# Optimization experiments

Hardware: AMD Instinct MI355X
Metric: run time of the kernel (lower is better)

The kernel has to match this reference:

```python
import jax, jax.numpy as jnp
import numpy as np

N_INST = 64
H, W_SP = 200, 320


def setup_inputs() -> dict:
    key = jax.random.key(0)
    ks = jax.random.split(key, 10)
    mask = jax.random.normal(ks[0], (1, N_INST, H, W_SP), dtype=jnp.float32)
    # class indices must lie in [1, 80]
    cls_idx = jax.random.randint(ks[1], (N_INST,), 0, 80, dtype=jnp.int32) + 1
    # rois: [batch_idx, xmin, ymin, xmax, ymax] with positive w, h
    xmin = jax.random.uniform(ks[2], (N_INST,), dtype=jnp.float32) * 800.0
    ymin = jax.random.uniform(ks[3], (N_INST,), dtype=jnp.float32) * 600.0
    bw = jax.random.uniform(ks[4], (N_INST,), dtype=jnp.float32) * 200.0 + 2.0
    bh = jax.random.uniform(ks[5], (N_INST,), dtype=jnp.float32) * 200.0 + 2.0
    bbox = jnp.stack([jnp.zeros(N_INST, jnp.float32), xmin, ymin, xmin + bw - 1.0, ymin + bh - 1.0], axis=1)
    # parameters (kaiming-ish scaling)
    U_w = jax.random.normal(ks[6], (256, 80), dtype=jnp.float32) * (2.0 / 80.0) ** 0.5
    V_w = jax.random.normal(ks[7], (256, 80), dtype=jnp.float32) * (2.0 / 80.0) ** 0.5
    Wc_w = jax.random.normal(ks[8], (128, 4), dtype=jnp.float32) * (2.0 / 4.0) ** 0.5
    P_w = jax.random.normal(ks[9], (1, 384), dtype=jnp.float32) * (2.0 / 384.0) ** 0.5
    return {"mask": mask, "bbox": bbox, "cls_idx": cls_idx,
            "U_w": U_w, "V_w": V_w, "Wc_w": Wc_w, "P_w": P_w}


def _position_matrix(rois):
    xmin, ymin, xmax, ymax = rois[:, 1], rois[:, 2], rois[:, 3], rois[:, 4]
    w = xmax - xmin + 1.0
    h = ymax - ymin + 1.0
    x_ctr = xmin + 0.5 * w
    y_ctr = ymin + 0.5 * h
    dx = -(x_ctr[:, None] - x_ctr[None, :]) / w[:, None]
    dy = -(y_ctr[:, None] - y_ctr[None, :]) / h[:, None]
    dw = jnp.log(w[None, :] / w[:, None])
    dh = jnp.log(h[None, :] / h[:, None])
    return jnp.stack([dx, dy, dw, dh], axis=2)  # (N, N, 4)


def reference(mask, bbox, cls_idx, U_w, V_w, Wc_w, P_w):
    n = cls_idx.shape[0]
    onehot = (cls_idx[:, None] - 1 == jnp.arange(80)[None, :]).astype(jnp.float32)  # (N, 80)
    feat1 = jax.nn.relu(onehot @ U_w.T)  # (N, 256)
    feat2 = jax.nn.relu(onehot @ V_w.T)  # (N, 256)
    cls_rel = feat1[:, None, :] * feat2[None, :, :]  # (N, N, 256)
    bbox_mat = _position_matrix(bbox)  # (N, N, 4)
    bbox_feat = jax.nn.relu(jnp.einsum('ijc,oc->ijo', bbox_mat, Wc_w))  # (N, N, 128)
    feat = jnp.concatenate([cls_rel, bbox_feat], axis=2)  # (N, N, 384)
    logit = jnp.einsum('ijc,c->ij', feat, P_w[0])  # 1x1 conv to scalar
    R = jax.nn.sigmoid(logit)
    O = jax.nn.relu(R - R.T)  # (N, N)
    trans_mask = jax.nn.sigmoid(mask)  # (1, N, H, W)
    # overlap[0,i] = mask[0,i]*trans_mask[0,i] * sum_j O[i,j]*trans_mask[0,j]
    weighted = jnp.einsum('ij,bjhw->bihw', O, trans_mask)
    new_mask = mask - mask * trans_mask * weighted
    return new_mask, O
```

## Files before the change

### kernel.cpp

```cpp
#include <hip/hip_runtime.h>
#include <math.h>

#define N_INST 64
#define HW 64000
#define TP 64
#define MASK_BLOCKS (HW / TP)

__device__ __forceinline__ float sigmoidf_(float x) {
    return 1.0f / (1.0f + __expf(-x));
}


__global__ void k_gather(const int* __restrict__ cls,
                         const float* __restrict__ U_w,
                         const float* __restrict__ V_w,
                         const float* __restrict__ P_w,
                         float* __restrict__ Afp,
                         float* __restrict__ BfT) {
    const int b = blockIdx.x;
    const int tid = threadIdx.x;
    const int cb = cls[b] - 1;
    float u = U_w[tid * 80 + cb];
    Afp[b * 256 + tid] = fmaxf(u, 0.0f) * P_w[tid];
    const int c = b * 4 + (tid >> 6);
    const int j = tid & 63;
    const int cj = cls[j] - 1;
    float v = V_w[c * 80 + cj];
    BfT[c * 64 + j] = fmaxf(v, 0.0f);
}

__global__ __launch_bounds__(64) void k_pair(const float* __restrict__ bbox,
                                             const float* __restrict__ Afp,
                                             const float* __restrict__ BfT,
                                             const float* __restrict__ Wc_w,
                                             const float* __restrict__ P_w,
                                             float* __restrict__ logit) {
    const int i = blockIdx.x;
    const int j = threadIdx.x;

    const float* __restrict__ ai = Afp + i * 256;
    float acc = 0.0f;
#pragma unroll 16
    for (int c = 0; c < 256; ++c) {
        acc = fmaf(ai[c], BfT[c * 64 + j], acc);
    }

    float xmin_i = bbox[i * 5 + 1], ymin_i = bbox[i * 5 + 2];
    float xmax_i = bbox[i * 5 + 3], ymax_i = bbox[i * 5 + 4];
    float xmin_j = bbox[j * 5 + 1], ymin_j = bbox[j * 5 + 2];
    float xmax_j = bbox[j * 5 + 3], ymax_j = bbox[j * 5 + 4];
    float wi = xmax_i - xmin_i + 1.0f, hi = ymax_i - ymin_i + 1.0f;
    float wj = xmax_j - xmin_j + 1.0f, hj = ymax_j - ymin_j + 1.0f;
    float xci = xmin_i + 0.5f * wi, yci = ymin_i + 0.5f * hi;
    float xcj = xmin_j + 0.5f * wj, ycj = ymin_j + 0.5f * hj;
    float dx = -(xci - xcj) / wi;
    float dy = -(yci - ycj) / hi;
    float dw = __logf(wj / wi);
    float dh = __logf(hj / hi);

#pragma unroll 8
    for (int o = 0; o < 128; ++o) {
        float s = dx * Wc_w[o * 4 + 0] + dy * Wc_w[o * 4 + 1]
                + dw * Wc_w[o * 4 + 2] + dh * Wc_w[o * 4 + 3];
        s = fmaxf(s, 0.0f);
        acc = fmaf(s, P_w[256 + o], acc);
    }

    logit[i * 64 + j] = acc;
}

__global__ void k_relu_R(const float* __restrict__ logit,
                         float* __restrict__ O_out,
                         float* __restrict__ OT_ws) {
    const int idx = blockIdx.x * blockDim.x + threadIdx.x;
    const int i = idx >> 6;
    const int j = idx & 63;
    float r = sigmoidf_(logit[i * 64 + j]) - sigmoidf_(logit[j * 64 + i]);
    r = fmaxf(r, 0.0f);
    O_out[i * 64 + j] = r;
    OT_ws[j * 64 + i] = r;
}

__global__ __launch_bounds__(256) void k_mask(const float* __restrict__ mask,
                                              const float* __restrict__ OT,
                                              float* __restrict__ out) {
    __shared__ float t_lds[64][64];
    __shared__ float o_lds[64][64];
    const int tid = threadIdx.x;
    const int pbase = blockIdx.x * TP;

#pragma unroll
    for (int k = 0; k < 16; ++k) {
        int idx = k * 256 + tid;
        ((float*)o_lds)[idx] = OT[idx];
    }
    {
        const int j0 = tid >> 6;
        const int p  = tid & 63;
#pragma unroll
        for (int k = 0; k < 16; ++k) {
            int j = j0 * 16 + k;
            float m = mask[j * HW + pbase + p];
            t_lds[j][p] = sigmoidf_(m);
        }
    }
    __syncthreads();

    const int pg = tid & 15;
    const int ig = tid >> 4;
    float acc[4][4];
#pragma unroll
    for (int a = 0; a < 4; ++a)
#pragma unroll
        for (int b = 0; b < 4; ++b) acc[a][b] = 0.0f;

#pragma unroll 8
    for (int j = 0; j < 64; ++j) {
        float4 t4 = *(const float4*)&t_lds[j][pg * 4];
        float4 o4 = *(const float4*)&o_lds[j][ig * 4];
        acc[0][0] = fmaf(o4.x, t4.x, acc[0][0]);
        acc[0][1] = fmaf(o4.x, t4.y, acc[0][1]);
        acc[0][2] = fmaf(o4.x, t4.z, acc[0][2]);
        acc[0][3] = fmaf(o4.x, t4.w, acc[0][3]);
        acc[1][0] = fmaf(o4.y, t4.x, acc[1][0]);
        acc[1][1] = fmaf(o4.y, t4.y, acc[1][1]);
        acc[1][2] = fmaf(o4.y, t4.z, acc[1][2]);
        acc[1][3] = fmaf(o4.y, t4.w, acc[1][3]);
        acc[2][0] = fmaf(o4.z, t4.x, acc[2][0]);
        acc[2][1] = fmaf(o4.z, t4.y, acc[2][1]);
        acc[2][2] = fmaf(o4.z, t4.z, acc[2][2]);
        acc[2][3] = fmaf(o4.z, t4.w, acc[2][3]);
        acc[3][0] = fmaf(o4.w, t4.x, acc[3][0]);
        acc[3][1] = fmaf(o4.w, t4.y, acc[3][1]);
        acc[3][2] = fmaf(o4.w, t4.z, acc[3][2]);
        acc[3][3] = fmaf(o4.w, t4.w, acc[3][3]);
    }

#pragma unroll
    for (int a = 0; a < 4; ++a) {
        const int i = ig * 4 + a;
        float4 ti = *(const float4*)&t_lds[i][pg * 4];
        float4 mi = *(const float4*)(mask + (size_t)i * HW + pbase + pg * 4);
        float4 r;
        r.x = mi.x * (1.0f - ti.x * acc[a][0]);
        r.y = mi.y * (1.0f - ti.y * acc[a][1]);
        r.z = mi.z * (1.0f - ti.z * acc[a][2]);
        r.w = mi.w * (1.0f - ti.w * acc[a][3]);
        *(float4*)(out + (size_t)i * HW + pbase + pg * 4) = r;
    }
}

extern "C" void kernel_launch(void* const* d_in, const int* in_sizes, int n_in,
                              void* d_out, int out_size, void* d_ws, size_t ws_size,
                              hipStream_t stream) {
    const float* mask = (const float*)d_in[0];
    const float* bbox = (const float*)d_in[1];
    const int*   cls  = (const int*)d_in[2];
    const float* U_w  = (const float*)d_in[3];
    const float* V_w  = (const float*)d_in[4];
    const float* Wc_w = (const float*)d_in[5];
    const float* P_w  = (const float*)d_in[6];

    float* out_mask = (float*)d_out;
    float* out_O    = (float*)d_out + (size_t)N_INST * HW;

    float* ws    = (float*)d_ws;
    float* logit = ws;
    float* OT    = ws + 4096;
    float* Afp   = ws + 8192;
    float* BfT   = ws + 24576;

    k_gather<<<64, 256, 0, stream>>>(cls, U_w, V_w, P_w, Afp, BfT);
    k_pair<<<64, 64, 0, stream>>>(bbox, Afp, BfT, Wc_w, P_w, logit);
    k_relu_R<<<16, 256, 0, stream>>>(logit, out_O, OT);
    k_mask<<<MASK_BLOCKS, 256, 0, stream>>>(mask, OT, out_mask);
}
```

Baseline: 102.2 us.

## Fuse gather, pair logits and antisymmetric sigmoid into one kernel

Replaces three small kernels (class-feature gather, pairwise logit, sigmoid difference) with a single kernel. Each thread computes both logit(i,j) and logit(j,i) directly from U_w/V_w with scattered reads, and writes O and its transpose. This removes two launches and the workspace round-trips, at the cost of doubling the pairwise arithmetic and using uncoalesced weight reads.

```diff
diff --git a/kernel.cpp b/kernel.cpp
--- a/kernel.cpp
+++ b/kernel.cpp
@@ -11,38 +11,31 @@
 }
 
 
-__global__ void k_gather(const int* __restrict__ cls,
-                         const float* __restrict__ U_w,
-                         const float* __restrict__ V_w,
-                         const float* __restrict__ P_w,
-                         float* __restrict__ Afp,
-                         float* __restrict__ BfT) {
-    const int b = blockIdx.x;
-    const int tid = threadIdx.x;
-    const int cb = cls[b] - 1;
-    float u = U_w[tid * 80 + cb];
-    Afp[b * 256 + tid] = fmaxf(u, 0.0f) * P_w[tid];
-    const int c = b * 4 + (tid >> 6);
-    const int j = tid & 63;
-    const int cj = cls[j] - 1;
-    float v = V_w[c * 80 + cj];
-    BfT[c * 64 + j] = fmaxf(v, 0.0f);
-}
-
-__global__ __launch_bounds__(64) void k_pair(const float* __restrict__ bbox,
-                                             const float* __restrict__ Afp,
-                                             const float* __restrict__ BfT,
-                                             const float* __restrict__ Wc_w,
-                                             const float* __restrict__ P_w,
-                                             float* __restrict__ logit) {
+__global__ __launch_bounds__(64) void k_O(const float* __restrict__ bbox,
+                                          const int*   __restrict__ cls,
+                                          const float* __restrict__ U_w,
+                                          const float* __restrict__ V_w,
+                                          const float* __restrict__ Wc_w,
+                                          const float* __restrict__ P_w,
+                                          float* __restrict__ O_out,
+                                          float* __restrict__ OT_ws) {
     const int i = blockIdx.x;
     const int j = threadIdx.x;
+    const int ci = cls[i] - 1;
+    const int cj = cls[j] - 1;
 
-    const float* __restrict__ ai = Afp + i * 256;
-    float acc = 0.0f;
-#pragma unroll 16
+    float accIJ = 0.0f, accJI = 0.0f;
+#pragma unroll 8
     for (int c = 0; c < 256; ++c) {
-        acc = fmaf(ai[c], BfT[c * 64 + j], acc);
+        float p  = P_w[c];
+        float ui = U_w[c * 80 + ci];
+        float vi = V_w[c * 80 + ci];
+        float uj = U_w[c * 80 + cj];
+        float vj = V_w[c * 80 + cj];
+        float ai = fmaxf(ui, 0.0f) * p;
+        float aj = fmaxf(uj, 0.0f) * p;
+        accIJ = fmaf(ai, fmaxf(vj, 0.0f), accIJ);
+        accJI = fmaf(aj, fmaxf(vi, 0.0f), accJI);
     }
 
     float xmin_i = bbox[i * 5 + 1], ymin_i = bbox[i * 5 + 2];
@@ -53,30 +46,28 @@
     float wj = xmax_j - xmin_j + 1.0f, hj = ymax_j - ymin_j + 1.0f;
     float xci = xmin_i + 0.5f * wi, yci = ymin_i + 0.5f * hi;
     float xcj = xmin_j + 0.5f * wj, ycj = ymin_j + 0.5f * hj;
-    float dx = -(xci - xcj) / wi;
-    float dy = -(yci - ycj) / hi;
-    float dw = __logf(wj / wi);
-    float dh = __logf(hj / hi);
+
+    float dx_ij = -(xci - xcj) / wi;
+    float dy_ij = -(yci - ycj) / hi;
+    float dw_ij = __logf(wj / wi);
+    float dh_ij = __logf(hj / hi);
+    float dx_ji = -(xcj - xci) / wj;
+    float dy_ji = -(ycj - yci) / hj;
+    float dw_ji = __logf(wi / wj);
+    float dh_ji = __logf(hi / hj);
 
 #pragma unroll 8
     for (int o = 0; o < 128; ++o) {
-        float s = dx * Wc_w[o * 4 + 0] + dy * Wc_w[o * 4 + 1]
-                + dw * Wc_w[o * 4 + 2] + dh * Wc_w[o * 4 + 3];
-        s = fmaxf(s, 0.0f);
-        acc = fmaf(s, P_w[256 + o], acc);
+        float w0 = Wc_w[o * 4 + 0], w1 = Wc_w[o * 4 + 1];
+        float w2 = Wc_w[o * 4 + 2], w3 = Wc_w[o * 4 + 3];
+        float p  = P_w[256 + o];
+        float sij = dx_ij * w0 + dy_ij * w1 + dw_ij * w2 + dh_ij * w3;
+        float sji = dx_ji * w0 + dy_ji * w1 + dw_ji * w2 + dh_ji * w3;
+        accIJ = fmaf(fmaxf(sij, 0.0f), p, accIJ);
+        accJI = fmaf(fmaxf(sji, 0.0f), p, accJI);
     }
 
-    logit[i * 64 + j] = acc;
-}
-
-__global__ void k_relu_R(const float* __restrict__ logit,
-                         float* __restrict__ O_out,
-                         float* __restrict__ OT_ws) {
-    const int idx = blockIdx.x * blockDim.x + threadIdx.x;
-    const int i = idx >> 6;
-    const int j = idx & 63;
-    float r = sigmoidf_(logit[i * 64 + j]) - sigmoidf_(logit[j * 64 + i]);
-    r = fmaxf(r, 0.0f);
+    float r = fmaxf(sigmoidf_(accIJ) - sigmoidf_(accJI), 0.0f);
     O_out[i * 64 + j] = r;
     OT_ws[j * 64 + i] = r;
 }
@@ -164,14 +155,9 @@
     float* out_mask = (float*)d_out;
     float* out_O    = (float*)d_out + (size_t)N_INST * HW;
 
-    float* ws    = (float*)d_ws;
-    float* logit = ws;
-    float* OT    = ws + 4096;
-    float* Afp   = ws + 8192;
-    float* BfT   = ws + 24576;
+    float* ws = (float*)d_ws;
+    float* OT = ws;
 
-    k_gather<<<64, 256, 0, stream>>>(cls, U_w, V_w, P_w, Afp, BfT);
-    k_pair<<<64, 64, 0, stream>>>(bbox, Afp, BfT, Wc_w, P_w, logit);
-    k_relu_R<<<16, 256, 0, stream>>>(logit, out_O, OT);
+    k_O<<<64, 64, 0, stream>>>(bbox, cls, U_w, V_w, Wc_w, P_w, out_O, OT);
     k_mask<<<MASK_BLOCKS, 256, 0, stream>>>(mask, OT, out_mask);
 }
```

Result: slower. 111.2 us (+8.7%).

## Fuse sigmoid-difference into mask kernel and split pair reduction across four waves

Applied to the files above, without the earlier changes.

Removes the separate relu(R-R^T) kernel: every mask block now loads the raw logits into padded LDS and computes the transposed O matrix itself, with block 0 also writing O to the output. The pair kernel splits its 256-channel and 128-output reductions across four wavefronts and combines the partial sums through LDS. This saves one kernel launch and shortens the serial pair kernel. In exchange, each of the 1000 mask blocks redundantly computes 8192 sigmoids and takes an extra barrier.

```diff
diff --git a/kernel.cpp b/kernel.cpp
--- a/kernel.cpp
+++ b/kernel.cpp
@@ -29,20 +29,23 @@
     BfT[c * 64 + j] = fmaxf(v, 0.0f);
 }
 
-__global__ __launch_bounds__(64) void k_pair(const float* __restrict__ bbox,
-                                             const float* __restrict__ Afp,
-                                             const float* __restrict__ BfT,
-                                             const float* __restrict__ Wc_w,
-                                             const float* __restrict__ P_w,
-                                             float* __restrict__ logit) {
+__global__ __launch_bounds__(256) void k_pair(const float* __restrict__ bbox,
+                                              const float* __restrict__ Afp,
+                                              const float* __restrict__ BfT,
+                                              const float* __restrict__ Wc_w,
+                                              const float* __restrict__ P_w,
+                                              float* __restrict__ logit) {
+    __shared__ float part[4][64];
     const int i = blockIdx.x;
-    const int j = threadIdx.x;
+    const int j = threadIdx.x & 63;
+    const int w = threadIdx.x >> 6;
 
-    const float* __restrict__ ai = Afp + i * 256;
+    const float* __restrict__ ai = Afp + i * 256 + w * 64;
+    const float* __restrict__ bt = BfT + (w * 64) * 64;
     float acc = 0.0f;
 #pragma unroll 16
-    for (int c = 0; c < 256; ++c) {
-        acc = fmaf(ai[c], BfT[c * 64 + j], acc);
+    for (int c = 0; c < 64; ++c) {
+        acc = fmaf(ai[c], bt[c * 64 + j], acc);
     }
 
     float xmin_i = bbox[i * 5 + 1], ymin_i = bbox[i * 5 + 2];
@@ -58,33 +61,29 @@
     float dw = __logf(wj / wi);
     float dh = __logf(hj / hi);
 
+    const float* __restrict__ wc = Wc_w + w * 32 * 4;
+    const float* __restrict__ pg = P_w + 256 + w * 32;
 #pragma unroll 8
-    for (int o = 0; o < 128; ++o) {
-        float s = dx * Wc_w[o * 4 + 0] + dy * Wc_w[o * 4 + 1]
-                + dw * Wc_w[o * 4 + 2] + dh * Wc_w[o * 4 + 3];
+    for (int oo = 0; oo < 32; ++oo) {
+        float s = dx * wc[oo * 4 + 0] + dy * wc[oo * 4 + 1]
+                + dw * wc[oo * 4 + 2] + dh * wc[oo * 4 + 3];
         s = fmaxf(s, 0.0f);
-        acc = fmaf(s, P_w[256 + o], acc);
+        acc = fmaf(s, pg[oo], acc);
     }
 
-    logit[i * 64 + j] = acc;
-}
-
-__global__ void k_relu_R(const float* __restrict__ logit,
-                         float* __restrict__ O_out,
-                         float* __restrict__ OT_ws) {
-    const int idx = blockIdx.x * blockDim.x + threadIdx.x;
-    const int i = idx >> 6;
-    const int j = idx & 63;
-    float r = sigmoidf_(logit[i * 64 + j]) - sigmoidf_(logit[j * 64 + i]);
-    r = fmaxf(r, 0.0f);
-    O_out[i * 64 + j] = r;
-    OT_ws[j * 64 + i] = r;
+    part[w][j] = acc;
+    __syncthreads();
+    if (threadIdx.x < 64) {
+        logit[i * 64 + j] = part[0][j] + part[1][j] + part[2][j] + part[3][j];
+    }
 }
 
 __global__ __launch_bounds__(256) void k_mask(const float* __restrict__ mask,
-                                              const float* __restrict__ OT,
+                                              const float* __restrict__ logit,
+                                              float* __restrict__ O_out,
                                               float* __restrict__ out) {
     __shared__ float t_lds[64][64];
+    __shared__ float l_lds[64][65];
     __shared__ float o_lds[64][64];
     const int tid = threadIdx.x;
     const int pbase = blockIdx.x * TP;
@@ -92,7 +91,7 @@
 #pragma unroll
     for (int k = 0; k < 16; ++k) {
         int idx = k * 256 + tid;
-        ((float*)o_lds)[idx] = OT[idx];
+        l_lds[idx >> 6][idx & 63] = logit[idx];
     }
     {
         const int j0 = tid >> 6;
@@ -103,6 +102,19 @@
             float m = mask[j * HW + pbase + p];
             t_lds[j][p] = sigmoidf_(m);
         }
+    }
+    __syncthreads();
+
+    const bool write_O = (blockIdx.x == 0);
+#pragma unroll
+    for (int k = 0; k < 16; ++k) {
+        int idx = k * 256 + tid;
+        int jj = idx >> 6;
+        int ii = idx & 63;
+        float r = sigmoidf_(l_lds[ii][jj]) - sigmoidf_(l_lds[jj][ii]);
+        r = fmaxf(r, 0.0f);
+        o_lds[jj][ii] = r;
+        if (write_O) O_out[ii * 64 + jj] = r;
     }
     __syncthreads();
 
@@ -166,12 +178,10 @@
 
     float* ws    = (float*)d_ws;
     float* logit = ws;
-    float* OT    = ws + 4096;
-    float* Afp   = ws + 8192;
-    float* BfT   = ws + 24576;
+    float* Afp   = ws + 4096;
+    float* BfT   = ws + 20480;
 
     k_gather<<<64, 256, 0, stream>>>(cls, U_w, V_w, P_w, Afp, BfT);
-    k_pair<<<64, 64, 0, stream>>>(bbox, Afp, BfT, Wc_w, P_w, logit);
-    k_relu_R<<<16, 256, 0, stream>>>(logit, out_O, OT);
-    k_mask<<<MASK_BLOCKS, 256, 0, stream>>>(mask, OT, out_mask);
+    k_pair<<<64, 256, 0, stream>>>(bbox, Afp, BfT, Wc_w, P_w, logit);
+    k_mask<<<MASK_BLOCKS, 256, 0, stream>>>(mask, logit, out_O, out_mask);
 }
```

Measured after the change: 96.31 us. 5.8% less time.
